# Kernel tuning notes

Measured on AMD Instinct MI355X. Metric: run time of the kernel, lower is better.

Reference implementation:

```python
import jax, jax.numpy as jnp
import numpy as np

B, TQ, TK, D, DV = 16, 2048, 2048, 128, 128
MASK_VAL = -1000000.0

def setup_inputs() -> dict:
    key = jax.random.key(0)
    kq, kk, kv, kl = jax.random.split(key, 4)
    q = jax.random.normal(kq, (B, TQ, D), dtype=jnp.float32)
    k = jax.random.normal(kk, (B, TK, D), dtype=jnp.float32)
    v = jax.random.normal(kv, (B, TK, DV), dtype=jnp.float32)
    valid_lens = jax.random.randint(kl, (B,), 1, TK, dtype=jnp.int64)
    return {"q": q, "k": k, "v": v, "valid_lens": valid_lens}

def reference(q, k, v, valid_lens):
    d = q.shape[-1]
    # scores: [B, Tq, Tk]
    scores = jnp.einsum('bqd,bkd->bqk', q, k) / jnp.sqrt(jnp.asarray(d, q.dtype))
    # mask key positions >= valid_len (same per-batch length for every query row)
    mask = jnp.arange(scores.shape[-1])[None, None, :] < valid_lens[:, None, None]
    scores = jnp.where(mask, scores, jnp.asarray(MASK_VAL, scores.dtype))
    attn = jax.nn.softmax(scores, axis=-1)
    # dropout p=0.0 (eval mode) -> identity
    return jnp.einsum('bqk,bkv->bqv', attn, v)
```

## Files before the change

### kernel.cpp

```cpp
#include <hip/hip_runtime.h>
#include <math.h>

#define NB 16
#define TQ 2048
#define TK 2048
#define DD 128
#define DVV 128

constexpr int KTILE = 32;
constexpr int QTILE = 128;

typedef __attribute__((ext_vector_type(8))) _Float16 half8;
typedef __attribute__((ext_vector_type(16))) float f32x16;
typedef __attribute__((ext_vector_type(4))) float f32x4;

__device__ inline float fast_exp2(float x) { return __builtin_amdgcn_exp2f(x); }
__device__ inline void setprio1() { __builtin_amdgcn_s_setprio(1); }
__device__ inline void setprio0() { __builtin_amdgcn_s_setprio(0); }

__device__ inline unsigned pk2(float a, float b) {
    auto h = __builtin_amdgcn_cvt_pkrtz(a, b);
    unsigned u;
    __builtin_memcpy(&u, &h, 4);
    return u;
}

__device__ inline void glds16(const _Float16* g, _Float16* l) {
    __builtin_amdgcn_global_load_lds(
        (const __attribute__((address_space(1))) void*)g,
        (__attribute__((address_space(3))) void*)l, 16, 0, 0);
}

__global__ __launch_bounds__(256)
void repack(const float* __restrict__ kg, const float* __restrict__ vg,
            const int* __restrict__ vlg,
            _Float16* __restrict__ Kpk, _Float16* __restrict__ Vpk)
{
    const int bt = blockIdx.x;
    const int b = bt >> 6, t = bt & 63;
    if (t * KTILE >= vlg[b]) return;
    const int tid = threadIdx.x;

    __shared__ float Vlds[32][129];

    const float* kin = kg + ((size_t)b * TK + t * KTILE) * DD;
    _Float16* kout = Kpk + ((size_t)bt << 12);
#pragma unroll
    for (int pp = 0; pp < 2; ++pp) {
        int s = tid + pp * 256;
        int c = s >> 6, l = s & 63;
        int row = l & 31, d0 = c * 16 + (l >> 5) * 8;
        const float* ip = kin + row * DD + d0;
        float4 f0 = *(const float4*)ip;
        float4 f1 = *(const float4*)(ip + 4);
        half8 hh;
        hh[0] = (_Float16)f0.x; hh[1] = (_Float16)f0.y;
        hh[2] = (_Float16)f0.z; hh[3] = (_Float16)f0.w;
        hh[4] = (_Float16)f1.x; hh[5] = (_Float16)f1.y;
        hh[6] = (_Float16)f1.z; hh[7] = (_Float16)f1.w;
        *(half8*)(kout + (size_t)s * 8) = hh;
    }

    const float* vin = vg + ((size_t)b * TK + t * KTILE) * DVV;
#pragma unroll
    for (int pp = 0; pp < 4; ++pp) {
        int idx = tid + pp * 256;
        int r = idx >> 5, c4 = (idx & 31) * 4;
        float4 f = *(const float4*)(vin + r * DVV + c4);
        Vlds[r][c4 + 0] = f.x; Vlds[r][c4 + 1] = f.y;
        Vlds[r][c4 + 2] = f.z; Vlds[r][c4 + 3] = f.w;
    }
    __syncthreads();
    _Float16* vout = Vpk + ((size_t)bt << 12);
#pragma unroll
    for (int pp = 0; pp < 2; ++pp) {
        int s = tid + pp * 256;
        int sv = s >> 6, l = s & 63;
        int dv = (sv >> 1) * 32 + (l & 31);
        int k0 = (sv & 1) * 16 + (l >> 5) * 8;
        half8 hh;
#pragma unroll
        for (int j = 0; j < 8; ++j)
            hh[j] = (_Float16)Vlds[k0 + j][dv];
        *(half8*)(vout + (size_t)s * 8) = hh;
    }
}

__global__ __launch_bounds__(256, 3)
void attn_fwd(const float* __restrict__ qg,
              const _Float16* __restrict__ Kpk, const _Float16* __restrict__ Vpk,
              const int* __restrict__ vlg,
              float* __restrict__ outg, _Float16* __restrict__ wso,
              float* __restrict__ wsml, int nsplit, int tpb)
{
    __shared__ __align__(16) _Float16 smem[16384];

    const int tid  = threadIdx.x;
    const int wid  = tid >> 6;
    const int lane = tid & 63;
    const int l31  = lane & 31;
    const int hi   = lane >> 5;

    const int b     = blockIdx.x & (NB - 1);
    const int qbase = (blockIdx.x >> 4) * QTILE;
    const int sp    = blockIdx.y;

    const int VL  = vlg[b];
    const int nkt = (VL + KTILE - 1) / KTILE;
    const int t0  = sp * tpb;
    const int t1  = min(nkt, t0 + tpb);
    if (t0 >= t1) return;

    const _Float16* ktb = Kpk + ((size_t)(b * 64) << 12);
    const _Float16* vtb = Vpk + ((size_t)(b * 64) << 12);

    half8 qf[8];
    {
        const float scale = 0.08838834764831845f * 1.4426950408889634f;
        const float* qp = qg + (size_t)(b * TQ + qbase + wid * 32 + l31) * DD;
#pragma unroll
        for (int c = 0; c < 8; ++c) {
            int d0 = c * 16 + hi * 8;
            float4 f0 = *(const float4*)(qp + d0);
            float4 f1 = *(const float4*)(qp + d0 + 4);
            half8 tq;
            tq[0] = (_Float16)(f0.x * scale); tq[1] = (_Float16)(f0.y * scale);
            tq[2] = (_Float16)(f0.z * scale); tq[3] = (_Float16)(f0.w * scale);
            tq[4] = (_Float16)(f1.x * scale); tq[5] = (_Float16)(f1.y * scale);
            tq[6] = (_Float16)(f1.z * scale); tq[7] = (_Float16)(f1.w * scale);
            qf[c] = tq;
        }
    }

    auto STAGE = [&](int buf, int t) {
        const bool isK = wid < 2;
        const int hf = wid & 1;
        const _Float16* src = (isK ? ktb : vtb) + ((size_t)t << 12) + hf * 2048 + lane * 8;
        _Float16* dst = smem + (isK ? 0 : 8192) + buf * 4096 + hf * 2048;
#pragma unroll
        for (int u = 0; u < 4; ++u)
            glds16(src + u * 512, dst + u * 512);
    };

    float m_i = -INFINITY, l_i = 0.f;
    f32x16 o[4];
#pragma unroll
    for (int n = 0; n < 4; ++n)
#pragma unroll
        for (int r = 0; r < 16; ++r) o[n][r] = 0.f;

    STAGE(0, t0);
    int cur = 0;
    for (int t = t0; t < t1; ++t) {
        const int kb = t * KTILE;
        const bool pre = (t + 1 < t1);
        if (pre) STAGE(cur ^ 1, t + 1);

        if (pre) asm volatile("s_waitcnt vmcnt(4)\ns_barrier" ::: "memory");
        else     asm volatile("s_waitcnt vmcnt(0)\ns_barrier" ::: "memory");

        const _Float16* kbuf = smem + cur * 4096;
        const _Float16* vbuf = smem + 8192 + cur * 4096;

        f32x16 sc;
#pragma unroll
        for (int r = 0; r < 16; ++r) sc[r] = 0.f;
        setprio1();
#pragma unroll
        for (int c = 0; c < 8; ++c) {
            half8 kf = *(const half8*)(kbuf + c * 512 + lane * 8);
            sc = __builtin_amdgcn_mfma_f32_32x32x16_f16(kf, qf[c], sc, 0, 0, 0);
        }
        setprio0();

        if (kb + KTILE > VL) {
#pragma unroll
            for (int r = 0; r < 16; ++r) {
                int rowk = kb + (r & 3) + 8 * (r >> 2) + 4 * hi;
                if (rowk >= VL) sc[r] = -1e30f;
            }
        }

        float mx = sc[0];
#pragma unroll
        for (int r = 1; r < 16; ++r) mx = fmaxf(mx, sc[r]);
        mx = fmaxf(mx, __shfl_xor(mx, 32));

        const bool skip = __all(mx <= m_i + 8.0f);
        const float mnew = skip ? m_i : fmaxf(m_i, mx);

        float p[16];
        float sum = 0.f;
#pragma unroll
        for (int r = 0; r < 16; ++r) {
            p[r] = fast_exp2(sc[r] - mnew);
            sum += p[r];
        }
        sum += __shfl_xor(sum, 32);

        unsigned a0 = pk2(p[0],  p[1]),  a1 = pk2(p[2],  p[3]);
        unsigned a2 = pk2(p[4],  p[5]),  a3 = pk2(p[6],  p[7]);
        unsigned b0 = pk2(p[8],  p[9]),  b1 = pk2(p[10], p[11]);
        unsigned b2 = pk2(p[12], p[13]), b3 = pk2(p[14], p[15]);
        unsigned pa0 = __shfl_xor(a0, 32), pa1 = __shfl_xor(a1, 32);
        unsigned pa2 = __shfl_xor(a2, 32), pa3 = __shfl_xor(a3, 32);
        unsigned pb0 = __shfl_xor(b0, 32), pb1 = __shfl_xor(b1, 32);
        unsigned pb2 = __shfl_xor(b2, 32), pb3 = __shfl_xor(b3, 32);
        union PF { unsigned u[4]; half8 v; } pf0, pf1;
        pf0.u[0] = hi ? pa2 : a0;  pf0.u[1] = hi ? pa3 : a1;
        pf0.u[2] = hi ? a2  : pa0; pf0.u[3] = hi ? a3  : pa1;
        pf1.u[0] = hi ? pb2 : b0;  pf1.u[1] = hi ? pb3 : b1;
        pf1.u[2] = hi ? b2  : pb0; pf1.u[3] = hi ? b3  : pb1;

        if (skip) {
            l_i += sum;
        } else {
            const float corr = fast_exp2(m_i - mnew);
            l_i = l_i * corr + sum;
            m_i = mnew;
#pragma unroll
            for (int n = 0; n < 4; ++n)
#pragma unroll
                for (int r = 0; r < 16; ++r) o[n][r] *= corr;
        }

        setprio1();
#pragma unroll
        for (int n = 0; n < 4; ++n) {
            half8 v0 = *(const half8*)(vbuf + (n * 2 + 0) * 512 + lane * 8);
            o[n] = __builtin_amdgcn_mfma_f32_32x32x16_f16(v0, pf0.v, o[n], 0, 0, 0);
            half8 v1 = *(const half8*)(vbuf + (n * 2 + 1) * 512 + lane * 8);
            o[n] = __builtin_amdgcn_mfma_f32_32x32x16_f16(v1, pf1.v, o[n], 0, 0, 0);
        }
        setprio0();

        asm volatile("s_waitcnt lgkmcnt(0)\ns_barrier" ::: "memory");
        cur ^= 1;
    }

    const float inv = (nsplit == 1) ? (1.0f / l_i) : 1.0f;
    float* tp = (float*)smem + wid * 1056;
#pragma unroll
    for (int n = 0; n < 4; ++n) {
#pragma unroll
        for (int r = 0; r < 16; ++r) {
            int row = (r & 3) + 8 * (r >> 2) + 4 * hi;
            tp[l31 * 33 + row] = o[n][r] * inv;
        }
        asm volatile("s_waitcnt lgkmcnt(0)" ::: "memory");
        if (nsplit == 1) {
            float* op = outg + (size_t)(b * TQ + qbase + wid * 32) * DVV + n * 32 + l31;
#pragma unroll
            for (int rr = 0; rr < 16; ++rr) {
                int qq = rr * 2 + hi;
                op[(size_t)qq * DVV] = tp[qq * 33 + l31];
            }
        } else {
            _Float16* po = wso + ((size_t)(sp * NB + b) * TQ + qbase + wid * 32) * DVV
                           + n * 32 + l31;
#pragma unroll
            for (int rr = 0; rr < 16; ++rr) {
                int qq = rr * 2 + hi;
                po[(size_t)qq * DVV] = (_Float16)tp[qq * 33 + l31];
            }
        }
        asm volatile("s_waitcnt lgkmcnt(0)" ::: "memory");
    }
    if (nsplit > 1 && hi == 0) {
        int q = qbase + wid * 32 + l31;
        *(float2*)&wsml[((size_t)(sp * NB + b) * TQ + q) * 2] = make_float2(m_i, l_i);
    }
}

__global__ __launch_bounds__(256)
void attn_combine(const _Float16* __restrict__ wso, const float* __restrict__ wsml,
                  const int* __restrict__ vlg, float* __restrict__ outg, int tpb)
{
    const int idx = blockIdx.x * 256 + threadIdx.x;
    const int d8 = idx & 15;
    const int q  = (idx >> 4) & (TQ - 1);
    const int b  = idx >> 15;

    const int VL  = vlg[b];
    const int nkt = (VL + KTILE - 1) / KTILE;
    const int nv  = (nkt + tpb - 1) / tpb;

    float M = -1e30f, den = 0.f;
    float acc[8] = {0.f, 0.f, 0.f, 0.f, 0.f, 0.f, 0.f, 0.f};
    for (int s = 0; s < nv; ++s) {
        const size_t row = (size_t)(s * NB + b) * TQ + q;
        float2 ml = *(const float2*)&wsml[row * 2];
        float Mn = fmaxf(M, ml.x);
        float c  = fast_exp2(M - Mn);
        float w  = fast_exp2(ml.x - Mn);
        half8 ov = *(const half8*)&wso[row * DVV + d8 * 8];
#pragma unroll
        for (int j = 0; j < 8; ++j)
            acc[j] = acc[j] * c + (float)ov[j] * w;
        den = den * c + w * ml.y;
        M = Mn;
    }
    const float inv = 1.0f / den;
    float* op = outg + ((size_t)b * TQ + q) * DVV + d8 * 8;
    f32x4 r0 = {acc[0] * inv, acc[1] * inv, acc[2] * inv, acc[3] * inv};
    f32x4 r1 = {acc[4] * inv, acc[5] * inv, acc[6] * inv, acc[7] * inv};
    *(f32x4*)op = r0;
    *(f32x4*)(op + 4) = r1;
}

extern "C" void kernel_launch(void* const* d_in, const int* in_sizes, int n_in,
                              void* d_out, int out_size, void* d_ws, size_t ws_size,
                              hipStream_t stream) {
    const float* q  = (const float*)d_in[0];
    const float* k  = (const float*)d_in[1];
    const float* v  = (const float*)d_in[2];
    const int*   vl = (const int*)d_in[3];
    float* out = (float*)d_out;

    const size_t pk_elems  = (size_t)NB * 64 * 4096;
    const size_t pk_bytes  = 2 * pk_elems * sizeof(_Float16);
    const size_t o_elems   = (size_t)NB * TQ * DVV;
    const size_t per_split = o_elems * sizeof(_Float16)
                           + (size_t)NB * TQ * 2 * sizeof(float);

    int ns = 1;
    if      (ws_size >= pk_bytes + 8 * per_split) ns = 8;
    else if (ws_size >= pk_bytes + 4 * per_split) ns = 4;
    else if (ws_size >= pk_bytes + 2 * per_split) ns = 2;
    const int tpb = 64 / ns;

    _Float16* Kpk = (_Float16*)d_ws;
    _Float16* Vpk = Kpk + pk_elems;
    _Float16* wso = Vpk + pk_elems;
    float*   wsml = (float*)(wso + (size_t)ns * o_elems);

    hipLaunchKernelGGL(repack, dim3(NB * 64), dim3(256), 0, stream,
                       k, v, vl, Kpk, Vpk);

    dim3 grid(NB * (TQ / QTILE), ns);
    hipLaunchKernelGGL(attn_fwd, grid, dim3(256), 0, stream,
                       q, Kpk, Vpk, vl, out, wso, wsml, ns, tpb);

    if (ns > 1) {
        dim3 cgrid((NB * TQ * 16) / 256);
        hipLaunchKernelGGL(attn_combine, cgrid, dim3(256), 0, stream,
                           wso, wsml, vl, out, tpb);
    }
}
```

Before: 75.01 us.

## Double query tile to 256 rows with 8 waves, direct-store epilogue, tree reductions

Raises the query tile from 128 to 256 rows and the block to 512 threads, so each K/V tile staged in LDS feeds eight waves instead of four and each wave issues fewer staging loads. It also removes the s_setprio hints, turns the max and sum reductions into trees, and replaces the LDS-transpose epilogue with direct vectorized stores of the MFMA output rows. The larger block halves the grid size, which may reduce CU fill and occupancy for short valid lengths, and dropping the priority hints changes how waves are scheduled against each other.

```diff
diff --git a/kernel.cpp b/kernel.cpp
--- a/kernel.cpp
+++ b/kernel.cpp
@@ -8,15 +8,13 @@
 #define DVV 128
 
 constexpr int KTILE = 32;
-constexpr int QTILE = 128;
+constexpr int QTILE = 256;
 
 typedef __attribute__((ext_vector_type(8))) _Float16 half8;
 typedef __attribute__((ext_vector_type(16))) float f32x16;
 typedef __attribute__((ext_vector_type(4))) float f32x4;
 
 __device__ inline float fast_exp2(float x) { return __builtin_amdgcn_exp2f(x); }
-__device__ inline void setprio1() { __builtin_amdgcn_s_setprio(1); }
-__device__ inline void setprio0() { __builtin_amdgcn_s_setprio(0); }
 
 __device__ inline unsigned pk2(float a, float b) {
     auto h = __builtin_amdgcn_cvt_pkrtz(a, b);
@@ -86,7 +84,7 @@
     }
 }
 
-__global__ __launch_bounds__(256, 3)
+__global__ __launch_bounds__(512, 2)
 void attn_fwd(const float* __restrict__ qg,
               const _Float16* __restrict__ Kpk, const _Float16* __restrict__ Vpk,
               const int* __restrict__ vlg,
@@ -132,14 +130,13 @@
         }
     }
 
+    const int qtr = wid & 3;
     auto STAGE = [&](int buf, int t) {
-        const bool isK = wid < 2;
-        const int hf = wid & 1;
-        const _Float16* src = (isK ? ktb : vtb) + ((size_t)t << 12) + hf * 2048 + lane * 8;
-        _Float16* dst = smem + (isK ? 0 : 8192) + buf * 4096 + hf * 2048;
-#pragma unroll
-        for (int u = 0; u < 4; ++u)
-            glds16(src + u * 512, dst + u * 512);
+        const bool isK = wid < 4;
+        const _Float16* src = (isK ? ktb : vtb) + ((size_t)t << 12) + qtr * 1024 + lane * 8;
+        _Float16* dst = smem + (isK ? 0 : 8192) + buf * 4096 + qtr * 1024;
+        glds16(src, dst);
+        glds16(src + 512, dst + 512);
     };
 
     float m_i = -INFINITY, l_i = 0.f;
@@ -156,7 +153,7 @@
         const bool pre = (t + 1 < t1);
         if (pre) STAGE(cur ^ 1, t + 1);
 
-        if (pre) asm volatile("s_waitcnt vmcnt(4)\ns_barrier" ::: "memory");
+        if (pre) asm volatile("s_waitcnt vmcnt(2)\ns_barrier" ::: "memory");
         else     asm volatile("s_waitcnt vmcnt(0)\ns_barrier" ::: "memory");
 
         const _Float16* kbuf = smem + cur * 4096;
@@ -165,13 +162,11 @@
         f32x16 sc;
 #pragma unroll
         for (int r = 0; r < 16; ++r) sc[r] = 0.f;
-        setprio1();
 #pragma unroll
         for (int c = 0; c < 8; ++c) {
             half8 kf = *(const half8*)(kbuf + c * 512 + lane * 8);
             sc = __builtin_amdgcn_mfma_f32_32x32x16_f16(kf, qf[c], sc, 0, 0, 0);
         }
-        setprio0();
 
         if (kb + KTILE > VL) {
 #pragma unroll
@@ -181,21 +176,29 @@
             }
         }
 
-        float mx = sc[0];
-#pragma unroll
-        for (int r = 1; r < 16; ++r) mx = fmaxf(mx, sc[r]);
+        float m8[8];
+#pragma unroll
+        for (int r = 0; r < 8; ++r) m8[r] = fmaxf(sc[r], sc[r + 8]);
+        float m4[4];
+#pragma unroll
+        for (int r = 0; r < 4; ++r) m4[r] = fmaxf(m8[r], m8[r + 4]);
+        float mx = fmaxf(fmaxf(m4[0], m4[1]), fmaxf(m4[2], m4[3]));
         mx = fmaxf(mx, __shfl_xor(mx, 32));
 
         const bool skip = __all(mx <= m_i + 8.0f);
         const float mnew = skip ? m_i : fmaxf(m_i, mx);
 
         float p[16];
-        float sum = 0.f;
-#pragma unroll
-        for (int r = 0; r < 16; ++r) {
+#pragma unroll
+        for (int r = 0; r < 16; ++r)
             p[r] = fast_exp2(sc[r] - mnew);
-            sum += p[r];
-        }
+        float s8[8];
+#pragma unroll
+        for (int r = 0; r < 8; ++r) s8[r] = p[r] + p[r + 8];
+        float s4[4];
+#pragma unroll
+        for (int r = 0; r < 4; ++r) s4[r] = s8[r] + s8[r + 4];
+        float sum = (s4[0] + s4[1]) + (s4[2] + s4[3]);
         sum += __shfl_xor(sum, 32);
 
         unsigned a0 = pk2(p[0],  p[1]),  a1 = pk2(p[2],  p[3]);
@@ -224,7 +227,6 @@
                 for (int r = 0; r < 16; ++r) o[n][r] *= corr;
         }
 
-        setprio1();
 #pragma unroll
         for (int n = 0; n < 4; ++n) {
             half8 v0 = *(const half8*)(vbuf + (n * 2 + 0) * 512 + lane * 8);
@@ -232,43 +234,39 @@
             half8 v1 = *(const half8*)(vbuf + (n * 2 + 1) * 512 + lane * 8);
             o[n] = __builtin_amdgcn_mfma_f32_32x32x16_f16(v1, pf1.v, o[n], 0, 0, 0);
         }
-        setprio0();
 
         asm volatile("s_waitcnt lgkmcnt(0)\ns_barrier" ::: "memory");
         cur ^= 1;
     }
 
-    const float inv = (nsplit == 1) ? (1.0f / l_i) : 1.0f;
-    float* tp = (float*)smem + wid * 1056;
-#pragma unroll
-    for (int n = 0; n < 4; ++n) {
-#pragma unroll
-        for (int r = 0; r < 16; ++r) {
-            int row = (r & 3) + 8 * (r >> 2) + 4 * hi;
-            tp[l31 * 33 + row] = o[n][r] * inv;
-        }
-        asm volatile("s_waitcnt lgkmcnt(0)" ::: "memory");
-        if (nsplit == 1) {
-            float* op = outg + (size_t)(b * TQ + qbase + wid * 32) * DVV + n * 32 + l31;
-#pragma unroll
-            for (int rr = 0; rr < 16; ++rr) {
-                int qq = rr * 2 + hi;
-                op[(size_t)qq * DVV] = tp[qq * 33 + l31];
+    if (nsplit == 1) {
+        const float inv = 1.0f / l_i;
+        float* op = outg + (size_t)(b * TQ + qbase + wid * 32 + l31) * DVV;
+#pragma unroll
+        for (int n = 0; n < 4; ++n)
+#pragma unroll
+            for (int g = 0; g < 4; ++g) {
+                int d0 = n * 32 + g * 8 + hi * 4;
+                f32x4 vv = {o[n][g * 4 + 0] * inv, o[n][g * 4 + 1] * inv,
+                            o[n][g * 4 + 2] * inv, o[n][g * 4 + 3] * inv};
+                *(f32x4*)(op + d0) = vv;
             }
-        } else {
-            _Float16* po = wso + ((size_t)(sp * NB + b) * TQ + qbase + wid * 32) * DVV
-                           + n * 32 + l31;
-#pragma unroll
-            for (int rr = 0; rr < 16; ++rr) {
-                int qq = rr * 2 + hi;
-                po[(size_t)qq * DVV] = (_Float16)tp[qq * 33 + l31];
+    } else {
+        _Float16* po = wso + ((size_t)(sp * NB + b) * TQ + qbase + wid * 32 + l31) * DVV;
+#pragma unroll
+        for (int n = 0; n < 4; ++n)
+#pragma unroll
+            for (int g = 0; g < 4; ++g) {
+                int d0 = n * 32 + g * 8 + hi * 4;
+                union { unsigned u[2]; double d; } hv;
+                hv.u[0] = pk2(o[n][g * 4 + 0], o[n][g * 4 + 1]);
+                hv.u[1] = pk2(o[n][g * 4 + 2], o[n][g * 4 + 3]);
+                *(double*)(po + d0) = hv.d;
             }
-        }
-        asm volatile("s_waitcnt lgkmcnt(0)" ::: "memory");
-    }
-    if (nsplit > 1 && hi == 0) {
-        int q = qbase + wid * 32 + l31;
-        *(float2*)&wsml[((size_t)(sp * NB + b) * TQ + q) * 2] = make_float2(m_i, l_i);
+        if (hi == 0) {
+            int q = qbase + wid * 32 + l31;
+            *(float2*)&wsml[((size_t)(sp * NB + b) * TQ + q) * 2] = make_float2(m_i, l_i);
+        }
     }
 }
 
@@ -338,7 +336,7 @@
                        k, v, vl, Kpk, Vpk);
 
     dim3 grid(NB * (TQ / QTILE), ns);
-    hipLaunchKernelGGL(attn_fwd, grid, dim3(256), 0, stream,
+    hipLaunchKernelGGL(attn_fwd, grid, dim3(512), 0, stream,
                        q, Kpk, Vpk, vl, out, wso, wsml, ns, tpb);
 
     if (ns > 1) {
```

After: 90.18 us. 20.2% more time.
